# Optimization experiments

Measured on AMD Instinct MI355X. Metric: run time of the kernel, lower is better.

Reference implementation:

```python
import jax, jax.numpy as jnp
import numpy as np

B, S, H = 2, 2048, 2048
NH, NKV, D = 16, 4, 128      # heads, kv heads, head_dim
GROUPS = NH // NKV
WIN = 1024                    # sliding window
EPS = 1e-5
THETA = 10000.0
NEG = -1e9


def _rms_norm(x, w):
    # over last dim (head_dim)
    var = jnp.mean(x * x, axis=-1, keepdims=True)
    return x * jax.lax.rsqrt(var + EPS) * w


def _rotate_half(x):
    x1, x2 = jnp.split(x, 2, axis=-1)
    return jnp.concatenate([-x2, x1], axis=-1)


def _apply_rope(q, k, cos, sin):
    # q: [B,NH,S,D], k: [B,NKV,S,D], cos/sin: [B,S,D]
    c = cos[:, None, :, :]
    s = sin[:, None, :, :]
    q = q * c + _rotate_half(q) * s
    k = k * c + _rotate_half(k) * s
    return q, k


def setup_inputs() -> dict:
    key = jax.random.key(0)
    ks = jax.random.split(key, 8)
    std = 0.02
    hidden_states = jax.random.normal(ks[0], (B, S, H), dtype=jnp.float32)
    Wq = jax.random.normal(ks[1], (NH * D, H), dtype=jnp.float32) * std
    Wk = jax.random.normal(ks[2], (NKV * D, H), dtype=jnp.float32) * std
    Wv = jax.random.normal(ks[3], (NKV * D, H), dtype=jnp.float32) * std
    Wo = jax.random.normal(ks[4], (H, NH * D), dtype=jnp.float32) * std
    Wg = jax.random.normal(ks[5], (NH * D, H), dtype=jnp.float32) * std
    q_norm_w = jnp.ones((D,), dtype=jnp.float32)
    k_norm_w = jnp.ones((D,), dtype=jnp.float32)
    # RoPE tables
    inv_freq = 1.0 / (THETA ** (jnp.arange(0, D, 2, dtype=jnp.float32) / D))
    pos = jnp.arange(S, dtype=jnp.float32)
    freqs = jnp.einsum('s,d->sd', pos, inv_freq)          # [S, D/2]
    emb = jnp.concatenate([freqs, freqs], axis=-1)        # [S, D]
    cos = jnp.broadcast_to(jnp.cos(emb)[None], (B, S, D)).astype(jnp.float32)
    sin = jnp.broadcast_to(jnp.sin(emb)[None], (B, S, D)).astype(jnp.float32)
    i = jnp.arange(S)[:, None]
    j = jnp.arange(S)[None, :]
    allowed = (j <= i) & (i - j < WIN)
    attention_mask = jnp.where(allowed, 0.0, NEG).astype(jnp.float32)[None, None]  # [1,1,S,S]
    return {
        'hidden_states': hidden_states, 'cos': cos, 'sin': sin,
        'attention_mask': attention_mask,
        'Wq': Wq, 'Wk': Wk, 'Wv': Wv, 'Wo': Wo, 'Wg': Wg,
        'q_norm_w': q_norm_w, 'k_norm_w': k_norm_w,
    }


def reference(hidden_states, cos, sin, attention_mask, Wq, Wk, Wv, Wo, Wg, q_norm_w, k_norm_w):
    x = hidden_states                                  # [B,S,H]
    q = (x @ Wq.T).reshape(B, S, NH, D)
    k = (x @ Wk.T).reshape(B, S, NKV, D)
    v = (x @ Wv.T).reshape(B, S, NKV, D)
    gate = x @ Wg.T                                    # [B,S,NH*D]
    q = _rms_norm(q, q_norm_w)
    k = _rms_norm(k, k_norm_w)
    q = q.transpose(0, 2, 1, 3)                        # [B,NH,S,D]
    k = k.transpose(0, 2, 1, 3)                        # [B,NKV,S,D]
    v = v.transpose(0, 2, 1, 3)
    # local (sliding) attention layer -> RoPE applied
    q, k = _apply_rope(q, k, cos, sin)
    # GQA: repeat kv heads
    k = jnp.repeat(k, GROUPS, axis=1)                  # [B,NH,S,D]
    v = jnp.repeat(v, GROUPS, axis=1)
    scaling = D ** -0.5
    scores = jnp.einsum('bhqd,bhkd->bhqk', q, k) * scaling
    scores = scores + attention_mask                   # broadcast [1,1,S,S]
    probs = jax.nn.softmax(scores.astype(jnp.float32), axis=-1).astype(q.dtype)
    out = jnp.einsum('bhqk,bhkd->bhqd', probs, v)      # [B,NH,S,D]
    out = out.transpose(0, 2, 1, 3).reshape(B, S, NH * D)
    out = out * jax.nn.sigmoid(gate)
    return out @ Wo.T                                  # [B,S,H]
```

## Files before the change

### kernel.cpp

```cpp
#include <hip/hip_runtime.h>
#include <hip/hip_bf16.h>

#define B_    2
#define S_    2048
#define H_    2048
#define NH_   16
#define NKV_  4
#define D_    128
#define WIN_  1024

typedef __attribute__((ext_vector_type(8))) short short8;
typedef __attribute__((ext_vector_type(4))) float f32x4;

__device__ __forceinline__ void gl2lds16(const void* g, void* l) {
  __builtin_amdgcn_global_load_lds(
      (const __attribute__((address_space(1))) void*)g,
      (__attribute__((address_space(3))) void*)l, 16, 0, 0);
}

__device__ __forceinline__ unsigned short f2bf(float x) {
  union { float f; unsigned int u; } v; v.f = x;
  unsigned int r = v.u + 0x7fffu + ((v.u >> 16) & 1u);
  return (unsigned short)(r >> 16);
}
__device__ __forceinline__ float bf2f(unsigned short u) {
  union { unsigned int i; float f; } v; v.i = ((unsigned int)u) << 16; return v.f;
}
__device__ __forceinline__ unsigned short f2bf_c(float x) {
  __hip_bfloat16 h = __float2bfloat16(x);
  union { __hip_bfloat16 h; unsigned short u; } v; v.h = h; return v.u;
}

#define CVT_TOTAL 5767168L
__global__ __launch_bounds__(256) void convert_all(
    const float* __restrict__ hs, const float* __restrict__ wq,
    const float* __restrict__ wk, const float* __restrict__ wv,
    const float* __restrict__ wg, const float* __restrict__ wo,
    unsigned short* __restrict__ xb, unsigned short* __restrict__ wall,
    unsigned short* __restrict__ wob) {
  long i = (long)blockIdx.x * 256 + threadIdx.x;
  if (i >= CVT_TOTAL) return;
  const float4* src; ushort4* dst;
  if (i < 2097152)      { src = (const float4*)hs + i;                         dst = (ushort4*)xb + i; }
  else if (i < 3145728) { long j = i - 2097152; src = (const float4*)wq + j;   dst = (ushort4*)wall + j; }
  else if (i < 3407872) { long j = i - 3145728; src = (const float4*)wk + j;   dst = (ushort4*)wall + 1048576 + j; }
  else if (i < 3670016) { long j = i - 3407872; src = (const float4*)wv + j;   dst = (ushort4*)wall + 1310720 + j; }
  else if (i < 4718592) { long j = i - 3670016; src = (const float4*)wg + j;   dst = (ushort4*)wall + 1572864 + j; }
  else                  { long j = i - 4718592; src = (const float4*)wo + j;   dst = (ushort4*)wob + j; }
  float4 v = *src;
  ushort4 o; o.x = f2bf(v.x); o.y = f2bf(v.y); o.z = f2bf(v.z); o.w = f2bf(v.w);
  *dst = o;
}

#define VMCNT0 asm volatile("s_waitcnt vmcnt(0)" ::: "memory")
#define SBAR   asm volatile("s_barrier" ::: "memory")
#define SB0    __builtin_amdgcn_sched_barrier(0)

__global__ __launch_bounds__(512, 2) void gemm_qkvg(
    const unsigned short* __restrict__ A,
    const unsigned short* __restrict__ Bm,
    unsigned short* __restrict__ C)
{
  const int KQ = 2048, NQ = 5120;
  __shared__ unsigned short As[2][256 * 64];
  __shared__ unsigned short Bs[2][320 * 64];
  const int t = threadIdx.x;
  const int lane = t & 63;
  const int wave = t >> 6;
  const int quad = lane >> 4, rl = lane & 15;
  const int bid = blockIdx.y * 16 + blockIdx.x;
  const int xcd = bid & 7, q = bid >> 3;
  const int bm = ((xcd & 3) * 4 + (q & 3)) * 256;
  const int bn = ((xcd >> 2) * 8 + (q >> 2)) * 320;
  const int wm = (wave >> 2) * 128, wn = (wave & 3) * 80;
  const int wub = (t & ~63) * 8;

#define STAGE_A_(d, k0, rd) { int cc = (rd) * 512 + t; int row = cc >> 3;      \
    int lc = (cc & 7) ^ (row & 7);                                             \
    gl2lds16(A + (long)(bm + row) * KQ + (k0) + lc * 8,                        \
             &As[d][(rd) * 4096 + wub]); }
#define STAGE_B_(d, k0, rd) { int cc = (rd) * 512 + t; int row = cc >> 3;      \
    int lc = (cc & 7) ^ (row & 7);                                             \
    gl2lds16(Bm + (long)(bn + row) * KQ + (k0) + lc * 8,                       \
             &Bs[d][(rd) * 4096 + wub]); }
#define RD_B(dst, cb, kk) { _Pragma("unroll") for (int j = 0; j < 5; j++) {    \
    int row = wn + j * 16 + rl;                                                \
    dst[j] = *(const short8*)(&Bs[cb][row * 64 + ((((kk)*4+quad)^(row&7))*8)]); } }
#define RD_A(dst, cb, kk, f0) { _Pragma("unroll") for (int f = 0; f < 4; f++) {\
    int row = wm + ((f0) + f) * 16 + rl;                                       \
    dst[f] = *(const short8*)(&As[cb][row * 64 + ((((kk)*4+quad)^(row&7))*8)]); } }
#define MM(a_, b_, f0) { __builtin_amdgcn_s_setprio(1);                        \
    _Pragma("unroll") for (int f = 0; f < 4; f++)                              \
    _Pragma("unroll") for (int j = 0; j < 5; j++)                              \
      acc[(f0)+f][j] = __builtin_amdgcn_mfma_f32_16x16x32_bf16(                \
          a_[f], b_[j], acc[(f0)+f][j], 0, 0, 0);                              \
    __builtin_amdgcn_s_setprio(0); }

  f32x4 acc[8][5];
#pragma unroll
  for (int f = 0; f < 8; f++)
#pragma unroll
    for (int j = 0; j < 5; j++) acc[f][j] = (f32x4){0.f, 0.f, 0.f, 0.f};

  STAGE_B_(0, 0, 0); STAGE_B_(0, 0, 1); STAGE_B_(0, 0, 2);
  STAGE_B_(0, 0, 3); STAGE_B_(0, 0, 4);
  STAGE_A_(0, 0, 0); STAGE_A_(0, 0, 1);
  STAGE_A_(0, 0, 2); STAGE_A_(0, 0, 3);
  VMCNT0; SBAR;

  short8 afX[4], bfrX[5], afY[4], bfrY[5];

  for (int tk = 0; tk < 32; ++tk) {
    const int c = tk & 1, d = c ^ 1;
    const int nk0 = tk * 64 + 64;
    const bool hn = tk < 31;
    RD_B(bfrX, c, 0); RD_A(afX, c, 0, 0);
    if (hn) {
      STAGE_B_(d, nk0, 0); STAGE_B_(d, nk0, 1); STAGE_B_(d, nk0, 2);
      STAGE_B_(d, nk0, 3); STAGE_B_(d, nk0, 4);
      STAGE_A_(d, nk0, 0); STAGE_A_(d, nk0, 1);
      STAGE_A_(d, nk0, 2); STAGE_A_(d, nk0, 3);
    }
    RD_A(afY, c, 0, 4);
    SB0;
    MM(afX, bfrX, 0);
    RD_B(bfrY, c, 1); RD_A(afX, c, 1, 0);
    SB0;
    MM(afY, bfrX, 4);
    RD_A(afY, c, 1, 4);
    SB0;
    MM(afX, bfrY, 0);
    SB0;
    MM(afY, bfrY, 4);
    VMCNT0; SBAR;
  }

#pragma unroll
  for (int f = 0; f < 8; f++) {
    int row0 = bm + wm + f * 16 + quad * 4;
#pragma unroll
    for (int j = 0; j < 5; j++) {
      int col = bn + wn + j * 16 + rl;
#pragma unroll
      for (int r = 0; r < 4; r++)
        C[(long)(row0 + r) * NQ + col] = f2bf(acc[f][j][r]);
    }
  }
#undef STAGE_A_
#undef STAGE_B_
#undef RD_B
#undef RD_A
#undef MM
}

template <bool OUT_BF16>
__global__ __launch_bounds__(256) void gemm_bt(
    const unsigned short* __restrict__ A,
    const unsigned short* __restrict__ Bm,
    void* __restrict__ Cv, int M, int N, int K)
{
  __shared__ unsigned short Asl[128 * 64];
  __shared__ unsigned short Bsl[128 * 64];
  const int t = threadIdx.x;
  const int lane = t & 63, wave = t >> 6;
  const int quad = lane >> 4, rl = lane & 15;
  const int bm = blockIdx.x * 128, bn = blockIdx.y * 128;
  const int wm = (wave >> 1) * 64, wn = (wave & 1) * 64;
  const int ldsbase = (t & ~63) * 8;

  f32x4 acc[4][4];
#pragma unroll
  for (int i = 0; i < 4; i++)
#pragma unroll
    for (int j = 0; j < 4; j++) acc[i][j] = (f32x4){0.f, 0.f, 0.f, 0.f};

  for (int k0 = 0; k0 < K; k0 += 64) {
#pragma unroll
    for (int i = 0; i < 4; i++) {
      int tt = i * 256 + t;
      int row = tt >> 3;
      int lc = (tt & 7) ^ (row & 7);
      gl2lds16(A + (long)(bm + row) * K + k0 + lc * 8, Asl + i * 2048 + ldsbase);
      gl2lds16(Bm + (long)(bn + row) * K + k0 + lc * 8, Bsl + i * 2048 + ldsbase);
    }
    __syncthreads();
#pragma unroll
    for (int kk = 0; kk < 2; kk++) {
      short8 af[4], bfr[4];
#pragma unroll
      for (int i = 0; i < 4; i++) {
        int row = wm + i * 16 + rl;
        af[i] = *(const short8*)(Asl + row * 64 + (((kk * 4 + quad) ^ (row & 7)) * 8));
      }
#pragma unroll
      for (int j = 0; j < 4; j++) {
        int row = wn + j * 16 + rl;
        bfr[j] = *(const short8*)(Bsl + row * 64 + (((kk * 4 + quad) ^ (row & 7)) * 8));
      }
#pragma unroll
      for (int i = 0; i < 4; i++)
#pragma unroll
        for (int j = 0; j < 4; j++)
          acc[i][j] = __builtin_amdgcn_mfma_f32_16x16x32_bf16(af[i], bfr[j], acc[i][j], 0, 0, 0);
    }
    __syncthreads();
  }
#pragma unroll
  for (int i = 0; i < 4; i++) {
    int row0 = bm + wm + i * 16 + quad * 4;
#pragma unroll
    for (int j = 0; j < 4; j++) {
      int col = bn + wn + j * 16 + rl;
#pragma unroll
      for (int r = 0; r < 4; r++) {
        if (OUT_BF16)
          ((unsigned short*)Cv)[(long)(row0 + r) * N + col] = f2bf(acc[i][j][r]);
        else
          ((float*)Cv)[(long)(row0 + r) * N + col] = acc[i][j][r];
      }
    }
  }
}

__global__ __launch_bounds__(256) void pack_and_transpose(
    const unsigned short* __restrict__ qkvg,
    const float* __restrict__ cosb, const float* __restrict__ sinb,
    const float* __restrict__ qw, const float* __restrict__ kw,
    unsigned short* __restrict__ qb, unsigned short* __restrict__ kb,
    unsigned short* __restrict__ vt)
{
  __shared__ unsigned short tile[64][136];
  int t = threadIdx.x;
  if (blockIdx.x >= 20480) {
    int blk = blockIdx.x - 20480;
    int st = blk & 31, kv = (blk >> 5) & 3, b = blk >> 7;
    int s0 = st * 64;
#pragma unroll
    for (int i = 0; i < 4; i++) {
      int idx = i * 256 + t;
      int r = idx >> 4, c = (idx & 15) * 8;
      short8 v = *(const short8*)(qkvg + (long)(b * S_ + s0 + r) * 5120 + 2560 + kv * 128 + c);
      *(short8*)(&tile[r][c]) = v;
    }
    __syncthreads();
    long vo = (long)(b * NKV_ + kv) * 128;
#pragma unroll
    for (int i = 0; i < 8; i++) {
      int idx = i * 256 + t;
      int d = idx >> 4, sc = idx & 15;
      ushort4 o;
      o.x = tile[sc * 4 + 0][d]; o.y = tile[sc * 4 + 1][d];
      o.z = tile[sc * 4 + 2][d]; o.w = tile[sc * 4 + 3][d];
      *(ushort4*)(vt + (vo + d) * S_ + s0 + sc * 4) = o;
    }
    return;
  }
  int lane = t & 63, wave = t >> 6;
  long gw = (long)blockIdx.x * 4 + wave;
  int hu = (int)(gw % 20);
  long bs = gw / 20;
  int b = (int)(bs / S_);
  int s = (int)(bs % S_);
  const unsigned short* row = qkvg + bs * 5120;

  bool isq = hu < 16;
  const unsigned short* base = isq ? (row + hu * 128) : (row + 2048 + (hu - 16) * 128);
  float x1 = bf2f(base[lane]), x2 = bf2f(base[lane + 64]);
  float ss = x1 * x1 + x2 * x2;
#pragma unroll
  for (int m = 1; m < 64; m <<= 1) ss += __shfl_xor(ss, m, 64);
  float inv = rsqrtf(ss * (1.0f / 128.0f) + 1e-5f);
  const float* w = isq ? qw : kw;
  float n1 = x1 * inv * w[lane], n2 = x2 * inv * w[lane + 64];
  const float* cp = cosb + bs * 128;
  const float* sp = sinb + bs * 128;
  float o1 = n1 * cp[lane] - n2 * sp[lane];
  float o2 = n2 * cp[lane + 64] + n1 * sp[lane + 64];
  if (isq) {
    long o = ((long)(b * NH_ + hu) * S_ + s) * 128;
    qb[o + lane] = f2bf(o1); qb[o + lane + 64] = f2bf(o2);
  } else {
    long o = ((long)(b * NKV_ + (hu - 16)) * S_ + s) * 128;
    kb[o + lane] = f2bf(o1); kb[o + lane + 64] = f2bf(o2);
  }
}

#define KSTR 136
#define VSTR 72
#define PSTR 68
__global__ __launch_bounds__(256, 3) void attn_kernel(
    const unsigned short* __restrict__ qb,
    const unsigned short* __restrict__ kbuf,
    const unsigned short* __restrict__ vt,
    const unsigned short* __restrict__ qkvg,
    unsigned short* __restrict__ aout)
{
  __shared__ unsigned short Ks[64 * KSTR];
  __shared__ unsigned short Vs[128 * VSTR];
  __shared__ unsigned short Ps[4][16 * PSTR];
  int t = threadIdx.x, lane = t & 63, wave = t >> 6;
  int quad = lane >> 4, rl = lane & 15;
  int blk = blockIdx.x;
  int qt = 31 - (blk >> 5);
  int qu = blk & 3;
  int kv = (blk >> 2) & 3;
  int b  = (blk >> 4) & 1;
  int h = kv * 4 + wave;
  int q0 = qt * 64 + qu * 16;

  const unsigned short* qhead = qb + (((long)(b * NH_ + h)) * S_) * 128;
  short8 qf[4];
#pragma unroll
  for (int ks = 0; ks < 4; ks++)
    qf[ks] = *(const short8*)(qhead + (long)(q0 + rl) * 128 + ks * 32 + quad * 8);

  f32x4 oacc[8];
#pragma unroll
  for (int j = 0; j < 8; j++) oacc[j] = (f32x4){0.f, 0.f, 0.f, 0.f};
  float m_r[4], l_r[4];
#pragma unroll
  for (int r = 0; r < 4; r++) { m_r[r] = -1e9f; l_r[r] = 0.f; }

  const unsigned short* kbase_p = kbuf + ((long)(b * NKV_ + kv)) * S_ * 128;
  const unsigned short* vbase_p = vt + ((long)(b * NKV_ + kv)) * 128 * S_;
  int t_lo = qt - 16; if (t_lo < 0) t_lo = 0;

  int kr[4], kc[4], vr[4], vc[4];
#pragma unroll
  for (int i = 0; i < 4; i++) {
    int idx = i * 256 + t;
    kr[i] = idx >> 4; kc[i] = (idx & 15) * 8;
    vr[i] = idx >> 3; vc[i] = (idx & 7) * 8;
  }

  {
    int kb0 = t_lo * 64;
    short8 kv0[4], vv0[4];
#pragma unroll
    for (int i = 0; i < 4; i++) {
      kv0[i] = *(const short8*)(kbase_p + (long)(kb0 + kr[i]) * 128 + kc[i]);
      vv0[i] = *(const short8*)(vbase_p + (long)vr[i] * S_ + kb0 + vc[i]);
    }
#pragma unroll
    for (int i = 0; i < 4; i++) {
      *(short8*)(Ks + kr[i] * KSTR + kc[i]) = kv0[i];
      *(short8*)(Vs + vr[i] * VSTR + vc[i]) = vv0[i];
    }
  }
  __syncthreads();

  const float scale = 0.08838834764831845f * 1.4426950408889634f;
  for (int kt = t_lo; kt <= qt; ++kt) {
    int kb0 = kt * 64;
    short8 kpre[4], vpre[4];
    if (kt < qt) {
      int nb0 = kb0 + 64;
#pragma unroll
      for (int i = 0; i < 4; i++) {
        kpre[i] = *(const short8*)(kbase_p + (long)(nb0 + kr[i]) * 128 + kc[i]);
        vpre[i] = *(const short8*)(vbase_p + (long)vr[i] * S_ + nb0 + vc[i]);
      }
    }

    f32x4 sc[4];
    __builtin_amdgcn_s_setprio(1);
#pragma unroll
    for (int nt = 0; nt < 4; nt++) {
      f32x4 c0 = (f32x4){0.f, 0.f, 0.f, 0.f};
#pragma unroll
      for (int ks = 0; ks < 4; ks++) {
        short8 bfrag = *(const short8*)(Ks + (nt * 16 + rl) * KSTR + (ks * 4 + quad) * 8);
        c0 = __builtin_amdgcn_mfma_f32_16x16x32_bf16(qf[ks], bfrag, c0, 0, 0, 0);
      }
      sc[nt] = c0;
    }
    __builtin_amdgcn_s_setprio(0);

#pragma unroll
    for (int nt = 0; nt < 4; nt++)
#pragma unroll
      for (int r = 0; r < 4; r++) {
        int i_row = q0 + quad * 4 + r;
        int j_col = kb0 + nt * 16 + rl;
        bool ok = (j_col <= i_row) && (i_row - j_col < WIN_);
        sc[nt][r] = ok ? sc[nt][r] * scale : -1e9f;
      }

    float mx[4];
#pragma unroll
    for (int r = 0; r < 4; r++) {
      float m0 = fmaxf(fmaxf(sc[0][r], sc[1][r]), fmaxf(sc[2][r], sc[3][r]));
#pragma unroll
      for (int m = 1; m < 16; m <<= 1) m0 = fmaxf(m0, __shfl_xor(m0, m, 64));
      mx[r] = m0;
    }
    bool need = (mx[0] > m_r[0]) | (mx[1] > m_r[1]) |
                (mx[2] > m_r[2]) | (mx[3] > m_r[3]);
    if (__any(need)) {
#pragma unroll
      for (int r = 0; r < 4; r++) {
        float newm = fmaxf(m_r[r], mx[r]);
        float alpha = exp2f(m_r[r] - newm);
        l_r[r] *= alpha;
#pragma unroll
        for (int j = 0; j < 8; j++) oacc[j][r] *= alpha;
        m_r[r] = newm;
      }
    }
#pragma unroll
    for (int r = 0; r < 4; r++) {
      float p0 = exp2f(sc[0][r] - m_r[r]), p1 = exp2f(sc[1][r] - m_r[r]);
      float p2 = exp2f(sc[2][r] - m_r[r]), p3 = exp2f(sc[3][r] - m_r[r]);
      float rs = p0 + p1 + p2 + p3;
#pragma unroll
      for (int m = 1; m < 16; m <<= 1) rs += __shfl_xor(rs, m, 64);
      l_r[r] += rs;
      unsigned short* pw = &Ps[wave][(quad * 4 + r) * PSTR];
      pw[0 * 16 + rl] = f2bf_c(p0);
      pw[1 * 16 + rl] = f2bf_c(p1);
      pw[2 * 16 + rl] = f2bf_c(p2);
      pw[3 * 16 + rl] = f2bf_c(p3);
    }

    __builtin_amdgcn_s_setprio(1);
#pragma unroll
    for (int ks2 = 0; ks2 < 2; ks2++) {
      short8 af = *(const short8*)(&Ps[wave][rl * PSTR + (ks2 * 4 + quad) * 8]);
#pragma unroll
      for (int j = 0; j < 8; j++) {
        short8 bf2 = *(const short8*)(Vs + (j * 16 + rl) * VSTR + (ks2 * 4 + quad) * 8);
        oacc[j] = __builtin_amdgcn_mfma_f32_16x16x32_bf16(af, bf2, oacc[j], 0, 0, 0);
      }
    }
    __builtin_amdgcn_s_setprio(0);

    if (kt < qt) {
      __syncthreads();
#pragma unroll
      for (int i = 0; i < 4; i++) {
        *(short8*)(Ks + kr[i] * KSTR + kc[i]) = kpre[i];
        *(short8*)(Vs + vr[i] * VSTR + vc[i]) = vpre[i];
      }
      __syncthreads();
    }
  }

#pragma unroll
  for (int r = 0; r < 4; r++) {
    int s_idx = q0 + quad * 4 + r;
    float invl = 1.0f / l_r[r];
    long rowoff = (long)(b * S_ + s_idx);
    const unsigned short* gptr = qkvg + rowoff * 5120 + 3072 + h * 128;
    unsigned short* orow = aout + rowoff * 2048 + h * 128;
#pragma unroll
    for (int j = 0; j < 8; j++) {
      int d = j * 16 + rl;
      float o = oacc[j][r] * invl;
      float g = bf2f(gptr[d]);
      o = o / (1.0f + __expf(-g));
      orow[d] = f2bf_c(o);
    }
  }
}

extern "C" void kernel_launch(void* const* d_in, const int* in_sizes, int n_in,
                              void* d_out, int out_size, void* d_ws, size_t ws_size,
                              hipStream_t stream) {
  (void)in_sizes; (void)n_in; (void)out_size; (void)ws_size;
  const float* hs   = (const float*)d_in[0];
  const float* cosb = (const float*)d_in[1];
  const float* sinb = (const float*)d_in[2];
  const float* Wq = (const float*)d_in[4];
  const float* Wk = (const float*)d_in[5];
  const float* Wv = (const float*)d_in[6];
  const float* Wo = (const float*)d_in[7];
  const float* Wg = (const float*)d_in[8];
  const float* qw = (const float*)d_in[9];
  const float* kw = (const float*)d_in[10];
  float* out = (float*)d_out;

  char* ws = (char*)d_ws;
  unsigned short* Xb   = (unsigned short*)ws; ws += (size_t)4096 * 2048 * 2;
  unsigned short* Wall = (unsigned short*)ws; ws += (size_t)5120 * 2048 * 2;
  unsigned short* Wob  = (unsigned short*)ws; ws += (size_t)2048 * 2048 * 2;
  unsigned short* qkvg = (unsigned short*)ws; ws += (size_t)4096 * 5120 * 2;
  unsigned short* qb   = (unsigned short*)ws; ws += (size_t)B_ * NH_ * S_ * D_ * 2;
  unsigned short* kbuf = (unsigned short*)ws; ws += (size_t)B_ * NKV_ * S_ * D_ * 2;
  unsigned short* vtb  = (unsigned short*)ws; ws += (size_t)B_ * NKV_ * S_ * D_ * 2;
  unsigned short* aout = (unsigned short*)ws; ws += (size_t)4096 * 2048 * 2;

  convert_all<<<(int)((CVT_TOTAL + 255) / 256), 256, 0, stream>>>(
      hs, Wq, Wk, Wv, Wg, Wo, Xb, Wall, Wob);
  gemm_qkvg<<<dim3(16, 16), 512, 0, stream>>>(Xb, Wall, qkvg);
  pack_and_transpose<<<20736, 256, 0, stream>>>(qkvg, cosb, sinb, qw, kw, qb, kbuf, vtb);
  attn_kernel<<<1024, 256, 0, stream>>>(qb, kbuf, vtb, qkvg, aout);
  gemm_bt<false><<<dim3(32, 16), 256, 0, stream>>>(aout, Wob, (void*)out, 4096, 2048, 2048);
}
```

Baseline: 379.6 us.

## Swizzle attention K/V shared tiles, drop GEMM sched barriers and XCD block remap

The attention kernel's K and V shared-memory tiles drop their padded strides (136/72) for unpadded tiles with an XOR swizzle. The swizzle is applied to the global load column, so each thread stores contiguously to shared memory and the reads use precomputed swizzled offsets. This saves LDS space and aims to avoid bank conflicts. Separately, the QKV/gate GEMM loses its sched_barrier fences and its XCD-aware block remapping, which returns to plain blockIdx tiling and may hurt L2 locality and instruction interleaving.

```diff
diff --git a/kernel.cpp b/kernel.cpp
--- a/kernel.cpp
+++ b/kernel.cpp
@@ -54,7 +54,6 @@
 
 #define VMCNT0 asm volatile("s_waitcnt vmcnt(0)" ::: "memory")
 #define SBAR   asm volatile("s_barrier" ::: "memory")
-#define SB0    __builtin_amdgcn_sched_barrier(0)
 
 __global__ __launch_bounds__(512, 2) void gemm_qkvg(
     const unsigned short* __restrict__ A,
@@ -68,10 +67,7 @@
   const int lane = t & 63;
   const int wave = t >> 6;
   const int quad = lane >> 4, rl = lane & 15;
-  const int bid = blockIdx.y * 16 + blockIdx.x;
-  const int xcd = bid & 7, q = bid >> 3;
-  const int bm = ((xcd & 3) * 4 + (q & 3)) * 256;
-  const int bn = ((xcd >> 2) * 8 + (q >> 2)) * 320;
+  const int bm = blockIdx.x * 256, bn = blockIdx.y * 320;
   const int wm = (wave >> 2) * 128, wn = (wave & 3) * 80;
   const int wub = (t & ~63) * 8;
 
@@ -122,15 +118,11 @@
       STAGE_A_(d, nk0, 2); STAGE_A_(d, nk0, 3);
     }
     RD_A(afY, c, 0, 4);
-    SB0;
     MM(afX, bfrX, 0);
     RD_B(bfrY, c, 1); RD_A(afX, c, 1, 0);
-    SB0;
     MM(afY, bfrX, 4);
     RD_A(afY, c, 1, 4);
-    SB0;
     MM(afX, bfrY, 0);
-    SB0;
     MM(afY, bfrY, 4);
     VMCNT0; SBAR;
   }
@@ -285,8 +277,6 @@
   }
 }
 
-#define KSTR 136
-#define VSTR 72
 #define PSTR 68
 __global__ __launch_bounds__(256, 3) void attn_kernel(
     const unsigned short* __restrict__ qb,
@@ -295,11 +285,12 @@
     const unsigned short* __restrict__ qkvg,
     unsigned short* __restrict__ aout)
 {
-  __shared__ unsigned short Ks[64 * KSTR];
-  __shared__ unsigned short Vs[128 * VSTR];
+  __shared__ unsigned short Ks[64 * 128];
+  __shared__ unsigned short Vs[128 * 64];
   __shared__ unsigned short Ps[4][16 * PSTR];
   int t = threadIdx.x, lane = t & 63, wave = t >> 6;
   int quad = lane >> 4, rl = lane & 15;
+  int rl7 = rl & 7;
   int blk = blockIdx.x;
   int qt = 31 - (blk >> 5);
   int qu = blk & 3;
@@ -314,6 +305,16 @@
   for (int ks = 0; ks < 4; ks++)
     qf[ks] = *(const short8*)(qhead + (long)(q0 + rl) * 128 + ks * 32 + quad * 8);
 
+  int kph[4], vph[2];
+#pragma unroll
+  for (int ks = 0; ks < 4; ks++) {
+    int L = ks * 4 + quad;
+    kph[ks] = (L & 8) | ((L & 7) ^ rl7);
+  }
+#pragma unroll
+  for (int ks2 = 0; ks2 < 2; ks2++)
+    vph[ks2] = (ks2 * 4 + quad) ^ rl7;
+
   f32x4 oacc[8];
 #pragma unroll
   for (int j = 0; j < 8; j++) oacc[j] = (f32x4){0.f, 0.f, 0.f, 0.f};
@@ -325,12 +326,14 @@
   const unsigned short* vbase_p = vt + ((long)(b * NKV_ + kv)) * 128 * S_;
   int t_lo = qt - 16; if (t_lo < 0) t_lo = 0;
 
-  int kr[4], kc[4], vr[4], vc[4];
+  int kr[4], kgc[4], vr[4], vgc[4];
 #pragma unroll
   for (int i = 0; i < 4; i++) {
     int idx = i * 256 + t;
-    kr[i] = idx >> 4; kc[i] = (idx & 15) * 8;
-    vr[i] = idx >> 3; vc[i] = (idx & 7) * 8;
+    kr[i] = idx >> 4;
+    { int p = idx & 15; kgc[i] = ((p & 8) | ((p & 7) ^ (kr[i] & 7))) * 8; }
+    vr[i] = idx >> 3;
+    { int p = idx & 7;  vgc[i] = (p ^ (vr[i] & 7)) * 8; }
   }
 
   {
@@ -338,13 +341,13 @@
     short8 kv0[4], vv0[4];
 #pragma unroll
     for (int i = 0; i < 4; i++) {
-      kv0[i] = *(const short8*)(kbase_p + (long)(kb0 + kr[i]) * 128 + kc[i]);
-      vv0[i] = *(const short8*)(vbase_p + (long)vr[i] * S_ + kb0 + vc[i]);
+      kv0[i] = *(const short8*)(kbase_p + (long)(kb0 + kr[i]) * 128 + kgc[i]);
+      vv0[i] = *(const short8*)(vbase_p + (long)vr[i] * S_ + kb0 + vgc[i]);
     }
 #pragma unroll
     for (int i = 0; i < 4; i++) {
-      *(short8*)(Ks + kr[i] * KSTR + kc[i]) = kv0[i];
-      *(short8*)(Vs + vr[i] * VSTR + vc[i]) = vv0[i];
+      *(short8*)(Ks + (i * 256 + t) * 8) = kv0[i];
+      *(short8*)(Vs + (i * 256 + t) * 8) = vv0[i];
     }
   }
   __syncthreads();
@@ -357,8 +360,8 @@
       int nb0 = kb0 + 64;
 #pragma unroll
       for (int i = 0; i < 4; i++) {
-        kpre[i] = *(const short8*)(kbase_p + (long)(nb0 + kr[i]) * 128 + kc[i]);
-        vpre[i] = *(const short8*)(vbase_p + (long)vr[i] * S_ + nb0 + vc[i]);
+        kpre[i] = *(const short8*)(kbase_p + (long)(nb0 + kr[i]) * 128 + kgc[i]);
+        vpre[i] = *(const short8*)(vbase_p + (long)vr[i] * S_ + nb0 + vgc[i]);
       }
     }
 
@@ -369,7 +372,7 @@
       f32x4 c0 = (f32x4){0.f, 0.f, 0.f, 0.f};
 #pragma unroll
       for (int ks = 0; ks < 4; ks++) {
-        short8 bfrag = *(const short8*)(Ks + (nt * 16 + rl) * KSTR + (ks * 4 + quad) * 8);
+        short8 bfrag = *(const short8*)(Ks + (nt * 16 + rl) * 128 + kph[ks] * 8);
         c0 = __builtin_amdgcn_mfma_f32_16x16x32_bf16(qf[ks], bfrag, c0, 0, 0, 0);
       }
       sc[nt] = c0;
@@ -428,7 +431,7 @@
       short8 af = *(const short8*)(&Ps[wave][rl * PSTR + (ks2 * 4 + quad) * 8]);
 #pragma unroll
       for (int j = 0; j < 8; j++) {
-        short8 bf2 = *(const short8*)(Vs + (j * 16 + rl) * VSTR + (ks2 * 4 + quad) * 8);
+        short8 bf2 = *(const short8*)(Vs + (j * 16 + rl) * 64 + vph[ks2] * 8);
         oacc[j] = __builtin_amdgcn_mfma_f32_16x16x32_bf16(af, bf2, oacc[j], 0, 0, 0);
       }
     }
@@ -438,8 +441,8 @@
       __syncthreads();
 #pragma unroll
       for (int i = 0; i < 4; i++) {
-        *(short8*)(Ks + kr[i] * KSTR + kc[i]) = kpre[i];
-        *(short8*)(Vs + vr[i] * VSTR + vc[i]) = vpre[i];
+        *(short8*)(Ks + (i * 256 + t) * 8) = kpre[i];
+        *(short8*)(Vs + (i * 256 + t) * 8) = vpre[i];
       }
       __syncthreads();
     }
```

Result: no change. 376.1 us (-0.9%).
